# Kernel optimization log

Hardware: AMD Instinct MI355X
Metric: run time of the kernel (lower is better)

## Reference

```python
import jax, jax.numpy as jnp
import numpy as np

E = 512; H = 512; L = 3; NH = 8; HD = H // NH; V = 32000
B = 64; S = 64; T = 20


def setup_inputs() -> dict:
    key = jax.random.key(0)
    ks = jax.random.split(key, 14)
    sc = 0.02
    return {
        "encoder_out": jax.random.normal(ks[0], (B, S, H), jnp.float32),
        "captions": jax.random.randint(ks[1], (B, T), 0, V),
        "embed_table": jax.random.normal(ks[2], (V, E), jnp.float32) * sc,
        "w_ih": jax.random.normal(ks[3], (L, 3 * H, E), jnp.float32) * sc,
        "w_hh": jax.random.normal(ks[4], (L, 3 * H, H), jnp.float32) * sc,
        "b_ih": jax.random.normal(ks[5], (L, 3 * H), jnp.float32) * sc,
        "b_hh": jax.random.normal(ks[6], (L, 3 * H), jnp.float32) * sc,
        "in_proj_w": jax.random.normal(ks[7], (3 * H, H), jnp.float32) * sc,
        "in_proj_b": jax.random.normal(ks[8], (3 * H,), jnp.float32) * sc,
        "out_proj_w": jax.random.normal(ks[9], (H, H), jnp.float32) * sc,
        "out_proj_b": jax.random.normal(ks[10], (H,), jnp.float32) * sc,
        "fc_w": jax.random.normal(ks[11], (V, H), jnp.float32) * sc,
        "fc_b": jax.random.normal(ks[12], (V,), jnp.float32) * sc,
    }


def _gru_cell(x, h, Wih, Whh, bih, bhh):
    # PyTorch GRUCell math. x: (B, in), h: (B, H)
    gi = x @ Wih.T + bih  # (B, 3H)
    gh = h @ Whh.T + bhh
    i_r, i_z, i_n = jnp.split(gi, 3, axis=-1)
    h_r, h_z, h_n = jnp.split(gh, 3, axis=-1)
    r = jax.nn.sigmoid(i_r + h_r)
    z = jax.nn.sigmoid(i_z + h_z)
    n = jnp.tanh(i_n + r * h_n)
    return (1.0 - z) * n + z * h


def reference(encoder_out, captions, embed_table, w_ih, w_hh, b_ih, b_hh,
              in_proj_w, in_proj_b, out_proj_w, out_proj_b, fc_w, fc_b):
    Wq, Wk, Wv = jnp.split(in_proj_w, 3, axis=0)
    bq, bk, bv = jnp.split(in_proj_b, 3, axis=0)
    # K/V projections of encoder_out are timestep-invariant: precompute once.
    Kh = (encoder_out @ Wk.T + bk).reshape(B, S, NH, HD)
    Vh = (encoder_out @ Wv.T + bv).reshape(B, S, NH, HD)
    scale = 1.0 / jnp.sqrt(jnp.float32(HD))

    emb = embed_table[captions]              # (B, T, E)
    xs = jnp.transpose(emb, (1, 0, 2))       # (T, B, E)

    def step(h, x_t):
        # h: (L, B, H); x_t: (B, E)
        new_h = []
        inp = x_t
        for l in range(L):
            hl = _gru_cell(inp, h[l], w_ih[l], w_hh[l], b_ih[l], b_hh[l])
            new_h.append(hl)
            inp = hl
        q = (inp @ Wq.T + bq).reshape(B, NH, HD)
        scores = jnp.einsum('bnd,bsnd->bns', q, Kh) * scale
        attn = jax.nn.softmax(scores, axis=-1)
        ctx = jnp.einsum('bns,bsnd->bnd', attn, Vh).reshape(B, H)
        ao = ctx @ out_proj_w.T + out_proj_b
        logits = ao @ fc_w.T + fc_b           # (B, V)
        return jnp.stack(new_h), logits

    h0 = jnp.zeros((L, B, H), dtype=encoder_out.dtype)
    _, logits = jax.lax.scan(step, h0, xs)    # logits: (T, B, V)
    return jnp.transpose(logits, (1, 0, 2))   # (B, T, V)
```

## Files before the change

### kernel.cpp

```cpp
#include <hip/hip_runtime.h>
#include <hip/hip_bf16.h>

#define TT 20
#define BB 64
#define SS 64
#define HH 512
#define EE 512
#define VV 32000

typedef __bf16 bf16x8 __attribute__((ext_vector_type(8)));
typedef float f32x4 __attribute__((ext_vector_type(4)));


__global__ __launch_bounds__(256) void f2bf_kernel(const float* __restrict__ in,
                                                   __hip_bfloat16* __restrict__ out, int n) {
    int i = blockIdx.x * 256 + threadIdx.x;
    if (i < n) out[i] = __float2bfloat16(in[i]);
}

__global__ __launch_bounds__(256) void zero_h_kernel(float* __restrict__ hf,
                                                     __hip_bfloat16* __restrict__ hb, int n) {
    int i = blockIdx.x * 256 + threadIdx.x;
    if (i < n) { hf[i] = 0.f; hb[i] = __float2bfloat16(0.f); }
}

__global__ __launch_bounds__(256) void gather_emb_kernel(const float* __restrict__ tab,
                                                         const int* __restrict__ cap,
                                                         __hip_bfloat16* __restrict__ out) {
    int i = blockIdx.x * 256 + threadIdx.x;
    int e = i & (EE - 1);
    int tb = i >> 9;
    int t = tb >> 6;
    int b = tb & 63;
    int tok = cap[b * TT + t];
    out[i] = __float2bfloat16(tab[(size_t)tok * EE + e]);
}


__global__ __launch_bounds__(256) void gemm_bt_kernel(
    const __hip_bfloat16* __restrict__ A,
    const __hip_bfloat16* __restrict__ Bm,
    const float* __restrict__ bias,
    float* __restrict__ Cf,
    __hip_bfloat16* __restrict__ Cb,
    int K, int ldc, int row_stride, int row_off,
    long sAz, long sBz, long sCz)
{
    A  += (size_t)blockIdx.z * sAz;
    Bm += (size_t)blockIdx.z * sBz;
    long cbase = (long)blockIdx.z * sCz;

    int m0 = blockIdx.x * 64, n0 = blockIdx.y * 64;
    int wave = threadIdx.x >> 6, lane = threadIdx.x & 63;
    int wm = wave & 1, wn = wave >> 1;
    int row16 = lane & 15, quad = lane >> 4;

    const __hip_bfloat16* a0p = A  + (size_t)(m0 + wm * 32 + row16) * K + quad * 8;
    const __hip_bfloat16* a1p = a0p + (size_t)16 * K;
    const __hip_bfloat16* b0p = Bm + (size_t)(n0 + wn * 32 + row16) * K + quad * 8;
    const __hip_bfloat16* b1p = b0p + (size_t)16 * K;

    f32x4 acc00 = {0.f, 0.f, 0.f, 0.f};
    f32x4 acc01 = {0.f, 0.f, 0.f, 0.f};
    f32x4 acc10 = {0.f, 0.f, 0.f, 0.f};
    f32x4 acc11 = {0.f, 0.f, 0.f, 0.f};

    for (int k = 0; k < K; k += 32) {
        bf16x8 a0 = *reinterpret_cast<const bf16x8*>(a0p + k);
        bf16x8 a1 = *reinterpret_cast<const bf16x8*>(a1p + k);
        bf16x8 b0 = *reinterpret_cast<const bf16x8*>(b0p + k);
        bf16x8 b1 = *reinterpret_cast<const bf16x8*>(b1p + k);
        acc00 = __builtin_amdgcn_mfma_f32_16x16x32_bf16(a0, b0, acc00, 0, 0, 0);
        acc01 = __builtin_amdgcn_mfma_f32_16x16x32_bf16(a0, b1, acc01, 0, 0, 0);
        acc10 = __builtin_amdgcn_mfma_f32_16x16x32_bf16(a1, b0, acc10, 0, 0, 0);
        acc11 = __builtin_amdgcn_mfma_f32_16x16x32_bf16(a1, b1, acc11, 0, 0, 0);
    }

    f32x4 accs[2][2] = {{acc00, acc01}, {acc10, acc11}};
#pragma unroll
    for (int mt = 0; mt < 2; ++mt) {
#pragma unroll
        for (int nt = 0; nt < 2; ++nt) {
            int col = n0 + wn * 32 + nt * 16 + row16;
            float bv = bias ? bias[col] : 0.f;
#pragma unroll
            for (int r = 0; r < 4; ++r) {
                int row = m0 + wm * 32 + mt * 16 + quad * 4 + r;
                long off = cbase + (long)(row * row_stride + row_off) * ldc + col;
                float v = accs[mt][nt][r] + bv;
                if (Cb) Cb[off] = __float2bfloat16(v);
                else    Cf[off] = v;
            }
        }
    }
}


__device__ inline float sigmf(float x) { return 1.f / (1.f + __expf(-x)); }

__global__ __launch_bounds__(256) void gru_combine_kernel(
    const float* __restrict__ GI, const float* __restrict__ GH,
    const float* __restrict__ bih, const float* __restrict__ bhh,
    float* __restrict__ h, __hip_bfloat16* __restrict__ hb)
{
    int i = blockIdx.x * 256 + threadIdx.x;
    int b = i >> 9, j = i & 511;
    const float* gi = GI + (size_t)b * 1536;
    const float* gh = GH + (size_t)b * 1536;
    float ir = gi[j]        + bih[j];
    float iz = gi[j + 512]  + bih[j + 512];
    float in_ = gi[j + 1024] + bih[j + 1024];
    float hr = gh[j]        + bhh[j];
    float hz = gh[j + 512]  + bhh[j + 512];
    float hn = gh[j + 1024] + bhh[j + 1024];
    float r = sigmf(ir + hr);
    float z = sigmf(iz + hz);
    float n = tanhf(in_ + r * hn);
    float hv = h[i];
    float hnew = (1.f - z) * n + z * hv;
    h[i] = hnew;
    hb[i] = __float2bfloat16(hnew);
}

__global__ __launch_bounds__(64) void attn_kernel(
    const float* __restrict__ q, const float* __restrict__ KV,
    __hip_bfloat16* __restrict__ ctxb)
{
    int b = blockIdx.x >> 3, nh = blockIdx.x & 7;
    int lane = threadIdx.x;

    const float* qrow = q + (size_t)b * HH + nh * 64;
    const float* kr   = KV + (size_t)(b * 64 + lane) * 1024 + nh * 64;
    float sc = 0.f;
#pragma unroll
    for (int d = 0; d < 64; ++d) sc += qrow[d] * kr[d];
    sc *= 0.125f;

    float m = sc;
    for (int off = 32; off; off >>= 1) m = fmaxf(m, __shfl_xor(m, off, 64));
    float e = __expf(sc - m);
    float s = e;
    for (int off = 32; off; off >>= 1) s += __shfl_xor(s, off, 64);
    float p = e / s;

    __shared__ float pl[64];
    pl[lane] = p;
    __syncthreads();

    float acc = 0.f;
    const float* vb = KV + (size_t)(b * 64) * 1024 + 512 + nh * 64 + lane;
#pragma unroll
    for (int si = 0; si < 64; ++si) acc += pl[si] * vb[(size_t)si * 1024];

    ctxb[(size_t)b * HH + nh * 64 + lane] = __float2bfloat16(acc);
}


extern "C" void kernel_launch(void* const* d_in, const int* in_sizes, int n_in,
                              void* d_out, int out_size, void* d_ws, size_t ws_size,
                              hipStream_t stream) {
    const float* enc        = (const float*)d_in[0];
    const int*   cap        = (const int*)d_in[1];
    const float* emb_tab    = (const float*)d_in[2];
    const float* w_ih       = (const float*)d_in[3];
    const float* w_hh       = (const float*)d_in[4];
    const float* b_ih       = (const float*)d_in[5];
    const float* b_hh       = (const float*)d_in[6];
    const float* in_proj_w  = (const float*)d_in[7];
    const float* in_proj_b  = (const float*)d_in[8];
    const float* out_proj_w = (const float*)d_in[9];
    const float* out_proj_b = (const float*)d_in[10];
    const float* fc_w       = (const float*)d_in[11];
    const float* fc_b       = (const float*)d_in[12];
    float* out = (float*)d_out;

    char* p = (char*)d_ws;
    auto alloc = [&](size_t bytes) {
        char* r = p;
        p += (bytes + 255) & ~(size_t)255;
        return r;
    };
    __hip_bfloat16* fcw_bf  = (__hip_bfloat16*)alloc((size_t)VV * HH * 2);
    __hip_bfloat16* enc_bf  = (__hip_bfloat16*)alloc((size_t)BB * SS * HH * 2);
    __hip_bfloat16* inp_bf  = (__hip_bfloat16*)alloc((size_t)1536 * 512 * 2);
    __hip_bfloat16* wih_bf  = (__hip_bfloat16*)alloc((size_t)3 * 1536 * 512 * 2);
    __hip_bfloat16* whh_bf  = (__hip_bfloat16*)alloc((size_t)3 * 1536 * 512 * 2);
    __hip_bfloat16* wo_bf   = (__hip_bfloat16*)alloc((size_t)512 * 512 * 2);
    __hip_bfloat16* xemb_bf = (__hip_bfloat16*)alloc((size_t)TT * BB * EE * 2);
    float* KV    = (float*)alloc((size_t)4096 * 1024 * 4);
    float* GI0   = (float*)alloc((size_t)1280 * 1536 * 4);
    float* GH    = (float*)alloc((size_t)3 * 64 * 1536 * 4);
    float* GIbuf = (float*)alloc((size_t)64 * 1536 * 4);
    float* hf    = (float*)alloc((size_t)3 * 64 * 512 * 4);
    __hip_bfloat16* hb     = (__hip_bfloat16*)alloc((size_t)3 * 64 * 512 * 2);
    float* qbuf  = (float*)alloc((size_t)64 * 512 * 4);
    __hip_bfloat16* ctx_bf = (__hip_bfloat16*)alloc((size_t)64 * 512 * 2);
    __hip_bfloat16* AO     = (__hip_bfloat16*)alloc((size_t)1280 * 512 * 2);

    auto cvt = [&](const float* src, __hip_bfloat16* dst, int n) {
        f2bf_kernel<<<(n + 255) / 256, 256, 0, stream>>>(src, dst, n);
    };
    cvt(fc_w, fcw_bf, VV * HH);
    cvt(enc, enc_bf, BB * SS * HH);
    cvt(in_proj_w, inp_bf, 1536 * 512);
    cvt(w_ih, wih_bf, 3 * 1536 * 512);
    cvt(w_hh, whh_bf, 3 * 1536 * 512);
    cvt(out_proj_w, wo_bf, 512 * 512);
    gather_emb_kernel<<<(TT * BB * EE) / 256, 256, 0, stream>>>(emb_tab, cap, xemb_bf);
    zero_h_kernel<<<(3 * 64 * 512) / 256, 256, 0, stream>>>(hf, hb, 3 * 64 * 512);

    gemm_bt_kernel<<<dim3(64, 16, 1), 256, 0, stream>>>(
        enc_bf, inp_bf + 512 * 512, in_proj_b + 512, KV, nullptr,
        512, 1024, 1, 0, 0, 0, 0);

    gemm_bt_kernel<<<dim3(20, 24, 1), 256, 0, stream>>>(
        xemb_bf, wih_bf, nullptr, GI0, nullptr,
        512, 1536, 1, 0, 0, 0, 0);

    for (int t = 0; t < TT; ++t) {
        gemm_bt_kernel<<<dim3(1, 24, 3), 256, 0, stream>>>(
            hb, whh_bf, nullptr, GH, nullptr,
            512, 1536, 1, 0, (long)64 * 512, (long)1536 * 512, (long)64 * 1536);

        gru_combine_kernel<<<128, 256, 0, stream>>>(
            GI0 + (size_t)t * 64 * 1536, GH, b_ih, b_hh, hf, hb);
        gemm_bt_kernel<<<dim3(1, 24, 1), 256, 0, stream>>>(
            hb, wih_bf + (size_t)1 * 1536 * 512, nullptr, GIbuf, nullptr,
            512, 1536, 1, 0, 0, 0, 0);
        gru_combine_kernel<<<128, 256, 0, stream>>>(
            GIbuf, GH + 64 * 1536, b_ih + 1536, b_hh + 1536, hf + 64 * 512, hb + 64 * 512);
        gemm_bt_kernel<<<dim3(1, 24, 1), 256, 0, stream>>>(
            hb + 64 * 512, wih_bf + (size_t)2 * 1536 * 512, nullptr, GIbuf, nullptr,
            512, 1536, 1, 0, 0, 0, 0);
        gru_combine_kernel<<<128, 256, 0, stream>>>(
            GIbuf, GH + 2 * 64 * 1536, b_ih + 2 * 1536, b_hh + 2 * 1536,
            hf + 2 * 64 * 512, hb + 2 * 64 * 512);

        gemm_bt_kernel<<<dim3(1, 8, 1), 256, 0, stream>>>(
            hb + 2 * 64 * 512, inp_bf, in_proj_b, qbuf, nullptr,
            512, 512, 1, 0, 0, 0, 0);

        attn_kernel<<<512, 64, 0, stream>>>(qbuf, KV, ctx_bf);

        gemm_bt_kernel<<<dim3(1, 8, 1), 256, 0, stream>>>(
            ctx_bf, wo_bf, out_proj_b, nullptr, AO,
            512, 512, TT, t, 0, 0, 0);
    }

    gemm_bt_kernel<<<dim3(20, 500, 1), 256, 0, stream>>>(
        AO, fcw_bf, fc_b, out, nullptr,
        512, VV, 1, 0, 0, 0, 0);
}
```

Measured before the change: 1.860 ms.

## Fuse recurrence into persistent grid-barrier kernel and add LDS-tiled 128x128 GEMM

Replaces the roughly 180 per-timestep kernel launches with a single persistent 64-block kernel. It loops over timesteps, uses an atomic grid barrier between stages, fuses each GRU gate GEMM with its elementwise combine, and overlaps the output projection with the next step's layer-0 work. The large GEMMs (KV projection, input gates, vocab projection) now use a new 128x128 tile kernel that stages operands through LDS with async global-to-LDS loads. This targets launch overhead and intermediate round trips through global memory. The cost is spin-wait barriers that depend on all 64 blocks being co-resident, and much less parallelism inside the recurrence.

```diff
diff --git a/kernel.cpp b/kernel.cpp
--- a/kernel.cpp
+++ b/kernel.cpp
@@ -3,13 +3,13 @@
 
 #define TT 20
 #define BB 64
-#define SS 64
 #define HH 512
-#define EE 512
 #define VV 32000
 
 typedef __bf16 bf16x8 __attribute__((ext_vector_type(8)));
 typedef float f32x4 __attribute__((ext_vector_type(4)));
+
+#define MFMA(a, b, c) __builtin_amdgcn_mfma_f32_16x16x32_bf16((a), (b), (c), 0, 0, 0)
 
 
 __global__ __launch_bounds__(256) void f2bf_kernel(const float* __restrict__ in,
@@ -18,141 +18,322 @@
     if (i < n) out[i] = __float2bfloat16(in[i]);
 }
 
-__global__ __launch_bounds__(256) void zero_h_kernel(float* __restrict__ hf,
-                                                     __hip_bfloat16* __restrict__ hb, int n) {
+__global__ __launch_bounds__(256) void init_kernel(float* __restrict__ hf,
+                                                   __hip_bfloat16* __restrict__ hb, int n,
+                                                   unsigned* __restrict__ barcnt) {
     int i = blockIdx.x * 256 + threadIdx.x;
     if (i < n) { hf[i] = 0.f; hb[i] = __float2bfloat16(0.f); }
+    if (i == 0) *barcnt = 0u;
 }
 
 __global__ __launch_bounds__(256) void gather_emb_kernel(const float* __restrict__ tab,
                                                          const int* __restrict__ cap,
                                                          __hip_bfloat16* __restrict__ out) {
     int i = blockIdx.x * 256 + threadIdx.x;
-    int e = i & (EE - 1);
+    int e = i & 511;
     int tb = i >> 9;
     int t = tb >> 6;
     int b = tb & 63;
     int tok = cap[b * TT + t];
-    out[i] = __float2bfloat16(tab[(size_t)tok * EE + e]);
-}
-
-
-__global__ __launch_bounds__(256) void gemm_bt_kernel(
+    out[i] = __float2bfloat16(tab[(size_t)tok * 512 + e]);
+}
+
+
+__device__ inline void async16(const void* g, void* l) {
+    __builtin_amdgcn_global_load_lds(
+        (const __attribute__((address_space(1))) unsigned int*)g,
+        (__attribute__((address_space(3))) unsigned int*)l, 16, 0, 0);
+}
+
+__global__ __launch_bounds__(256) void fastgemm_kernel(
     const __hip_bfloat16* __restrict__ A,
     const __hip_bfloat16* __restrict__ Bm,
     const float* __restrict__ bias,
-    float* __restrict__ Cf,
-    __hip_bfloat16* __restrict__ Cb,
-    int K, int ldc, int row_stride, int row_off,
-    long sAz, long sBz, long sCz)
+    float* __restrict__ C,
+    int K, int N)
 {
-    A  += (size_t)blockIdx.z * sAz;
-    Bm += (size_t)blockIdx.z * sBz;
-    long cbase = (long)blockIdx.z * sCz;
-
-    int m0 = blockIdx.x * 64, n0 = blockIdx.y * 64;
-    int wave = threadIdx.x >> 6, lane = threadIdx.x & 63;
+    __shared__ __align__(16) __hip_bfloat16 lsA[128 * 32];
+    __shared__ __align__(16) __hip_bfloat16 lsB[128 * 32];
+
+    int m0 = blockIdx.x * 128, n0 = blockIdx.y * 128;
+    int tid = threadIdx.x;
+    int wave = tid >> 6, lane = tid & 63, row16 = lane & 15, quad = lane >> 4;
     int wm = wave & 1, wn = wave >> 1;
-    int row16 = lane & 15, quad = lane >> 4;
-
-    const __hip_bfloat16* a0p = A  + (size_t)(m0 + wm * 32 + row16) * K + quad * 8;
-    const __hip_bfloat16* a1p = a0p + (size_t)16 * K;
-    const __hip_bfloat16* b0p = Bm + (size_t)(n0 + wn * 32 + row16) * K + quad * 8;
-    const __hip_bfloat16* b1p = b0p + (size_t)16 * K;
-
-    f32x4 acc00 = {0.f, 0.f, 0.f, 0.f};
-    f32x4 acc01 = {0.f, 0.f, 0.f, 0.f};
-    f32x4 acc10 = {0.f, 0.f, 0.f, 0.f};
-    f32x4 acc11 = {0.f, 0.f, 0.f, 0.f};
-
-    for (int k = 0; k < K; k += 32) {
-        bf16x8 a0 = *reinterpret_cast<const bf16x8*>(a0p + k);
-        bf16x8 a1 = *reinterpret_cast<const bf16x8*>(a1p + k);
-        bf16x8 b0 = *reinterpret_cast<const bf16x8*>(b0p + k);
-        bf16x8 b1 = *reinterpret_cast<const bf16x8*>(b1p + k);
-        acc00 = __builtin_amdgcn_mfma_f32_16x16x32_bf16(a0, b0, acc00, 0, 0, 0);
-        acc01 = __builtin_amdgcn_mfma_f32_16x16x32_bf16(a0, b1, acc01, 0, 0, 0);
-        acc10 = __builtin_amdgcn_mfma_f32_16x16x32_bf16(a1, b0, acc10, 0, 0, 0);
-        acc11 = __builtin_amdgcn_mfma_f32_16x16x32_bf16(a1, b1, acc11, 0, 0, 0);
-    }
-
-    f32x4 accs[2][2] = {{acc00, acc01}, {acc10, acc11}};
-#pragma unroll
-    for (int mt = 0; mt < 2; ++mt) {
-#pragma unroll
-        for (int nt = 0; nt < 2; ++nt) {
-            int col = n0 + wn * 32 + nt * 16 + row16;
+
+    int srow = tid >> 2;
+    int scol = (tid & 3) * 8;
+    const __hip_bfloat16* ga = A + (size_t)(m0 + srow) * K + scol;
+    const __hip_bfloat16* gb = Bm + (size_t)(n0 + srow) * K + scol;
+    __hip_bfloat16* la0 = &lsA[srow * 32 + scol];
+    __hip_bfloat16* la1 = &lsA[(64 + srow) * 32 + scol];
+    __hip_bfloat16* lb0 = &lsB[srow * 32 + scol];
+    __hip_bfloat16* lb1 = &lsB[(64 + srow) * 32 + scol];
+
+    f32x4 acc[4][4] = {};
+
+    for (int kt = 0; kt < K; kt += 32) {
+        async16(ga + kt, la0);
+        async16(ga + kt + (size_t)64 * K, la1);
+        async16(gb + kt, lb0);
+        async16(gb + kt + (size_t)64 * K, lb1);
+        __syncthreads();
+
+        bf16x8 af[4], bfr[4];
+#pragma unroll
+        for (int i = 0; i < 4; ++i)
+            af[i] = *(const bf16x8*)&lsA[(wm * 64 + i * 16 + row16) * 32 + quad * 8];
+#pragma unroll
+        for (int j = 0; j < 4; ++j)
+            bfr[j] = *(const bf16x8*)&lsB[(wn * 64 + j * 16 + row16) * 32 + quad * 8];
+#pragma unroll
+        for (int i = 0; i < 4; ++i)
+#pragma unroll
+            for (int j = 0; j < 4; ++j)
+                acc[i][j] = MFMA(af[i], bfr[j], acc[i][j]);
+        __syncthreads();
+    }
+
+#pragma unroll
+    for (int i = 0; i < 4; ++i)
+#pragma unroll
+        for (int j = 0; j < 4; ++j) {
+            int col = n0 + wn * 64 + j * 16 + row16;
             float bv = bias ? bias[col] : 0.f;
 #pragma unroll
             for (int r = 0; r < 4; ++r) {
-                int row = m0 + wm * 32 + mt * 16 + quad * 4 + r;
-                long off = cbase + (long)(row * row_stride + row_off) * ldc + col;
-                float v = accs[mt][nt][r] + bv;
-                if (Cb) Cb[off] = __float2bfloat16(v);
-                else    Cf[off] = v;
+                int row = m0 + wm * 64 + i * 16 + quad * 4 + r;
+                C[(size_t)row * N + col] = acc[i][j][r] + bv;
             }
         }
-    }
 }
 
 
 __device__ inline float sigmf(float x) { return 1.f / (1.f + __expf(-x)); }
 
-__global__ __launch_bounds__(256) void gru_combine_kernel(
-    const float* __restrict__ GI, const float* __restrict__ GH,
-    const float* __restrict__ bih, const float* __restrict__ bhh,
-    float* __restrict__ h, __hip_bfloat16* __restrict__ hb)
+struct RecArgs {
+    const __hip_bfloat16 *whh, *wih, *wq, *wo;
+    const float *bih, *bhh, *bq, *bo;
+    const float *GI0all;
+    const float *KV;
+    float *hf;
+    __hip_bfloat16 *hb;
+    float *qf;
+    __hip_bfloat16 *ctx;
+    __hip_bfloat16 *AO;
+    unsigned *barcnt;
+};
+
+#define NBLK 64u
+
+__device__ inline void gridbar(unsigned* cnt, unsigned target) {
+    __syncthreads();
+    if (threadIdx.x == 0) {
+        __threadfence();
+        __hip_atomic_fetch_add(cnt, 1u, __ATOMIC_RELAXED, __HIP_MEMORY_SCOPE_AGENT);
+        while (__hip_atomic_load(cnt, __ATOMIC_RELAXED, __HIP_MEMORY_SCOPE_AGENT) < target) {}
+        __threadfence();
+    }
+    __syncthreads();
+}
+
+__device__ inline void gru_stage_l0(
+    const float* __restrict__ GIt, const __hip_bfloat16* __restrict__ A_gh,
+    const __hip_bfloat16* __restrict__ Whh0,
+    const float* __restrict__ bih0, const float* __restrict__ bhh0,
+    const float* __restrict__ hf_in, float* __restrict__ hf_out,
+    __hip_bfloat16* __restrict__ hb_out,
+    int j0, int w, int row16, int quad)
 {
-    int i = blockIdx.x * 256 + threadIdx.x;
-    int b = i >> 9, j = i & 511;
-    const float* gi = GI + (size_t)b * 1536;
-    const float* gh = GH + (size_t)b * 1536;
-    float ir = gi[j]        + bih[j];
-    float iz = gi[j + 512]  + bih[j + 512];
-    float in_ = gi[j + 1024] + bih[j + 1024];
-    float hr = gh[j]        + bhh[j];
-    float hz = gh[j + 512]  + bhh[j + 512];
-    float hn = gh[j + 1024] + bhh[j + 1024];
-    float r = sigmf(ir + hr);
-    float z = sigmf(iz + hz);
-    float n = tanhf(in_ + r * hn);
-    float hv = h[i];
-    float hnew = (1.f - z) * n + z * hv;
-    h[i] = hnew;
-    hb[i] = __float2bfloat16(hnew);
-}
-
-__global__ __launch_bounds__(64) void attn_kernel(
-    const float* __restrict__ q, const float* __restrict__ KV,
-    __hip_bfloat16* __restrict__ ctxb)
+    int koff = quad * 8;
+    const __hip_bfloat16* ah = A_gh + (size_t)(w * 16 + row16) * 512 + koff;
+    const __hip_bfloat16* wh0 = Whh0 + (size_t)(j0 + row16) * 512 + koff;
+    const __hip_bfloat16* wh1 = wh0 + (size_t)512 * 512;
+    const __hip_bfloat16* wh2 = wh1 + (size_t)512 * 512;
+    f32x4 gh0 = {0,0,0,0}, gh1 = {0,0,0,0}, gh2 = {0,0,0,0};
+    for (int k = 0; k < 512; k += 32) {
+        bf16x8 av = *(const bf16x8*)(ah + k);
+        gh0 = MFMA(av, *(const bf16x8*)(wh0 + k), gh0);
+        gh1 = MFMA(av, *(const bf16x8*)(wh1 + k), gh1);
+        gh2 = MFMA(av, *(const bf16x8*)(wh2 + k), gh2);
+    }
+    int j = j0 + row16;
+    float br = bih0[j], bz = bih0[j + 512], bn = bih0[j + 1024];
+    float cr = bhh0[j], cz = bhh0[j + 512], cn = bhh0[j + 1024];
+#pragma unroll
+    for (int r = 0; r < 4; ++r) {
+        int b = w * 16 + quad * 4 + r;
+        float gir = GIt[(size_t)b * 1536 + j];
+        float giz = GIt[(size_t)b * 1536 + j + 512];
+        float gin = GIt[(size_t)b * 1536 + j + 1024];
+        float rg = sigmf(gir + br + gh0[r] + cr);
+        float zg = sigmf(giz + bz + gh1[r] + cz);
+        float ng = tanhf(gin + bn + rg * (gh2[r] + cn));
+        float hv = (1.f - zg) * ng + zg * hf_in[(size_t)b * 512 + j];
+        hf_out[(size_t)b * 512 + j] = hv;
+        hb_out[(size_t)b * 512 + j] = __float2bfloat16(hv);
+    }
+}
+
+__device__ inline void gru_stage_mid(
+    const __hip_bfloat16* __restrict__ A_gi, const __hip_bfloat16* __restrict__ A_gh,
+    const __hip_bfloat16* __restrict__ Wih_l, const __hip_bfloat16* __restrict__ Whh_l,
+    const float* __restrict__ bih_l, const float* __restrict__ bhh_l,
+    const float* __restrict__ hf_in, float* __restrict__ hf_out,
+    __hip_bfloat16* __restrict__ hb_out,
+    int j0, int w, int row16, int quad)
 {
-    int b = blockIdx.x >> 3, nh = blockIdx.x & 7;
-    int lane = threadIdx.x;
-
-    const float* qrow = q + (size_t)b * HH + nh * 64;
-    const float* kr   = KV + (size_t)(b * 64 + lane) * 1024 + nh * 64;
-    float sc = 0.f;
-#pragma unroll
-    for (int d = 0; d < 64; ++d) sc += qrow[d] * kr[d];
-    sc *= 0.125f;
-
-    float m = sc;
-    for (int off = 32; off; off >>= 1) m = fmaxf(m, __shfl_xor(m, off, 64));
-    float e = __expf(sc - m);
-    float s = e;
-    for (int off = 32; off; off >>= 1) s += __shfl_xor(s, off, 64);
-    float p = e / s;
-
-    __shared__ float pl[64];
-    pl[lane] = p;
-    __syncthreads();
-
-    float acc = 0.f;
-    const float* vb = KV + (size_t)(b * 64) * 1024 + 512 + nh * 64 + lane;
-#pragma unroll
-    for (int si = 0; si < 64; ++si) acc += pl[si] * vb[(size_t)si * 1024];
-
-    ctxb[(size_t)b * HH + nh * 64 + lane] = __float2bfloat16(acc);
+    int koff = quad * 8;
+    const __hip_bfloat16* ai = A_gi + (size_t)(w * 16 + row16) * 512 + koff;
+    const __hip_bfloat16* ah = A_gh + (size_t)(w * 16 + row16) * 512 + koff;
+    const __hip_bfloat16* wi0 = Wih_l + (size_t)(j0 + row16) * 512 + koff;
+    const __hip_bfloat16* wi1 = wi0 + (size_t)512 * 512;
+    const __hip_bfloat16* wi2 = wi1 + (size_t)512 * 512;
+    const __hip_bfloat16* wh0 = Whh_l + (size_t)(j0 + row16) * 512 + koff;
+    const __hip_bfloat16* wh1 = wh0 + (size_t)512 * 512;
+    const __hip_bfloat16* wh2 = wh1 + (size_t)512 * 512;
+    f32x4 gi0 = {0,0,0,0}, gi1 = {0,0,0,0}, gi2 = {0,0,0,0};
+    f32x4 gh0 = {0,0,0,0}, gh1 = {0,0,0,0}, gh2 = {0,0,0,0};
+    for (int k = 0; k < 512; k += 32) {
+        bf16x8 av_i = *(const bf16x8*)(ai + k);
+        bf16x8 av_h = *(const bf16x8*)(ah + k);
+        gi0 = MFMA(av_i, *(const bf16x8*)(wi0 + k), gi0);
+        gi1 = MFMA(av_i, *(const bf16x8*)(wi1 + k), gi1);
+        gi2 = MFMA(av_i, *(const bf16x8*)(wi2 + k), gi2);
+        gh0 = MFMA(av_h, *(const bf16x8*)(wh0 + k), gh0);
+        gh1 = MFMA(av_h, *(const bf16x8*)(wh1 + k), gh1);
+        gh2 = MFMA(av_h, *(const bf16x8*)(wh2 + k), gh2);
+    }
+    int j = j0 + row16;
+    float br = bih_l[j], bz = bih_l[j + 512], bn = bih_l[j + 1024];
+    float cr = bhh_l[j], cz = bhh_l[j + 512], cn = bhh_l[j + 1024];
+#pragma unroll
+    for (int r = 0; r < 4; ++r) {
+        int b = w * 16 + quad * 4 + r;
+        float rg = sigmf(gi0[r] + br + gh0[r] + cr);
+        float zg = sigmf(gi1[r] + bz + gh1[r] + cz);
+        float ng = tanhf(gi2[r] + bn + rg * (gh2[r] + cn));
+        float hv = (1.f - zg) * ng + zg * hf_in[(size_t)b * 512 + j];
+        hf_out[(size_t)b * 512 + j] = hv;
+        hb_out[(size_t)b * 512 + j] = __float2bfloat16(hv);
+    }
+}
+
+__device__ inline f32x4 proj16(const __hip_bfloat16* __restrict__ A,
+                               const __hip_bfloat16* __restrict__ Bw,
+                               int w, int row16, int quad)
+{
+    int koff = quad * 8;
+    const __hip_bfloat16* ap = A + (size_t)(w * 16 + row16) * 512 + koff;
+    const __hip_bfloat16* bp = Bw + (size_t)row16 * 512 + koff;
+    f32x4 acc = {0,0,0,0};
+    for (int k = 0; k < 512; k += 32)
+        acc = MFMA(*(const bf16x8*)(ap + k), *(const bf16x8*)(bp + k), acc);
+    return acc;
+}
+
+#define HSTATE (3 * 64 * 512)
+
+__global__ void __launch_bounds__(256, 1) recurrence_kernel(RecArgs a) {
+    const int tid = threadIdx.x;
+    const int blk = blockIdx.x;
+    const int w = tid >> 6, lane = tid & 63, row16 = lane & 15, quad = lane >> 4;
+    unsigned epoch = 0;
+
+    for (int t = 0; t < TT; ++t) {
+        const int cur = t & 1, nxt = cur ^ 1;
+        const __hip_bfloat16* hbc = a.hb + cur * HSTATE;
+        __hip_bfloat16* hbn = a.hb + nxt * HSTATE;
+        const float* hfc = a.hf + cur * HSTATE;
+        float* hfn = a.hf + nxt * HSTATE;
+
+        if (blk < 32) {
+            gru_stage_l0(a.GI0all + (size_t)t * 64 * 1536, hbc, a.whh,
+                         a.bih, a.bhh, hfc, hfn, hbn, blk * 16, w, row16, quad);
+        } else if (t > 0) {
+            int j0 = (blk - 32) * 16;
+            f32x4 acc = proj16(a.ctx, a.wo + (size_t)j0 * 512, w, row16, quad);
+            int j = j0 + row16;
+            float bv = a.bo[j];
+#pragma unroll
+            for (int r = 0; r < 4; ++r) {
+                int b = w * 16 + quad * 4 + r;
+                a.AO[(size_t)(b * TT + (t - 1)) * 512 + j] = __float2bfloat16(acc[r] + bv);
+            }
+        }
+        gridbar(a.barcnt, NBLK * ++epoch);
+
+        if (blk < 32)
+            gru_stage_mid(hbn, hbc + HSTATE / 3,
+                          a.wih + (size_t)1 * 1536 * 512, a.whh + (size_t)1 * 1536 * 512,
+                          a.bih + 1536, a.bhh + 1536,
+                          hfc + HSTATE / 3, hfn + HSTATE / 3, hbn + HSTATE / 3,
+                          blk * 16, w, row16, quad);
+        gridbar(a.barcnt, NBLK * ++epoch);
+
+        if (blk < 32)
+            gru_stage_mid(hbn + HSTATE / 3, hbc + 2 * (HSTATE / 3),
+                          a.wih + (size_t)2 * 1536 * 512, a.whh + (size_t)2 * 1536 * 512,
+                          a.bih + 2 * 1536, a.bhh + 2 * 1536,
+                          hfc + 2 * (HSTATE / 3), hfn + 2 * (HSTATE / 3),
+                          hbn + 2 * (HSTATE / 3),
+                          blk * 16, w, row16, quad);
+        gridbar(a.barcnt, NBLK * ++epoch);
+
+        if (blk < 32) {
+            int j0 = blk * 16;
+            f32x4 acc = proj16(hbn + 2 * (HSTATE / 3), a.wq + (size_t)j0 * 512, w, row16, quad);
+            int j = j0 + row16;
+            float bv = a.bq[j];
+#pragma unroll
+            for (int r = 0; r < 4; ++r) {
+                int b = w * 16 + quad * 4 + r;
+                a.qf[(size_t)b * 512 + j] = acc[r] + bv;
+            }
+        }
+        gridbar(a.barcnt, NBLK * ++epoch);
+
+        {
+            int wg = blk * 4 + w;
+#pragma unroll
+            for (int it = 0; it < 2; ++it) {
+                int task = wg * 2 + it;
+                int b = task >> 3, h = task & 7;
+                const float* qrow = a.qf + (size_t)b * 512 + h * 64;
+                const float* kr = a.KV + (size_t)(b * 64 + lane) * 1024 + h * 64;
+                float sc = 0.f;
+#pragma unroll
+                for (int d = 0; d < 64; ++d) sc += qrow[d] * kr[d];
+                sc *= 0.125f;
+                float m = sc;
+                for (int off = 32; off; off >>= 1) m = fmaxf(m, __shfl_xor(m, off, 64));
+                float e = __expf(sc - m);
+                float s = e;
+                for (int off = 32; off; off >>= 1) s += __shfl_xor(s, off, 64);
+                float p = e / s;
+                float accv = 0.f;
+                const float* vb = a.KV + (size_t)(b * 64) * 1024 + 512 + h * 64 + lane;
+#pragma unroll
+                for (int si = 0; si < 64; ++si) {
+                    float ps = __shfl(p, si, 64);
+                    accv += ps * vb[(size_t)si * 1024];
+                }
+                a.ctx[(size_t)b * 512 + h * 64 + lane] = __float2bfloat16(accv);
+            }
+        }
+        gridbar(a.barcnt, NBLK * ++epoch);
+    }
+
+    if (blk >= 32) {
+        int j0 = (blk - 32) * 16;
+        f32x4 acc = proj16(a.ctx, a.wo + (size_t)j0 * 512, w, row16, quad);
+        int j = j0 + row16;
+        float bv = a.bo[j];
+#pragma unroll
+        for (int r = 0; r < 4; ++r) {
+            int b = w * 16 + quad * 4 + r;
+            a.AO[(size_t)(b * TT + 19) * 512 + j] = __float2bfloat16(acc[r] + bv);
+        }
+    }
 }
 
 
@@ -181,73 +362,47 @@
         return r;
     };
     __hip_bfloat16* fcw_bf  = (__hip_bfloat16*)alloc((size_t)VV * HH * 2);
-    __hip_bfloat16* enc_bf  = (__hip_bfloat16*)alloc((size_t)BB * SS * HH * 2);
+    __hip_bfloat16* enc_bf  = (__hip_bfloat16*)alloc((size_t)64 * 64 * 512 * 2);
     __hip_bfloat16* inp_bf  = (__hip_bfloat16*)alloc((size_t)1536 * 512 * 2);
     __hip_bfloat16* wih_bf  = (__hip_bfloat16*)alloc((size_t)3 * 1536 * 512 * 2);
     __hip_bfloat16* whh_bf  = (__hip_bfloat16*)alloc((size_t)3 * 1536 * 512 * 2);
     __hip_bfloat16* wo_bf   = (__hip_bfloat16*)alloc((size_t)512 * 512 * 2);
-    __hip_bfloat16* xemb_bf = (__hip_bfloat16*)alloc((size_t)TT * BB * EE * 2);
-    float* KV    = (float*)alloc((size_t)4096 * 1024 * 4);
-    float* GI0   = (float*)alloc((size_t)1280 * 1536 * 4);
-    float* GH    = (float*)alloc((size_t)3 * 64 * 1536 * 4);
-    float* GIbuf = (float*)alloc((size_t)64 * 1536 * 4);
-    float* hf    = (float*)alloc((size_t)3 * 64 * 512 * 4);
-    __hip_bfloat16* hb     = (__hip_bfloat16*)alloc((size_t)3 * 64 * 512 * 2);
-    float* qbuf  = (float*)alloc((size_t)64 * 512 * 4);
+    __hip_bfloat16* xemb_bf = (__hip_bfloat16*)alloc((size_t)TT * 64 * 512 * 2);
+    float* KV     = (float*)alloc((size_t)4096 * 1024 * 4);
+    float* GI0all = (float*)alloc((size_t)1280 * 1536 * 4);
+    float* hf     = (float*)alloc((size_t)2 * HSTATE * 4);
+    __hip_bfloat16* hb = (__hip_bfloat16*)alloc((size_t)2 * HSTATE * 2);
+    float* qf     = (float*)alloc((size_t)64 * 512 * 4);
     __hip_bfloat16* ctx_bf = (__hip_bfloat16*)alloc((size_t)64 * 512 * 2);
     __hip_bfloat16* AO     = (__hip_bfloat16*)alloc((size_t)1280 * 512 * 2);
-
-    auto cvt = [&](const float* src, __hip_bfloat16* dst, int n) {
-        f2bf_kernel<<<(n + 255) / 256, 256, 0, stream>>>(src, dst, n);
+    unsigned* barcnt = (unsigned*)alloc(256);
+
+    auto cvt = [&](const float* src, __hip_bfloat16* dst, size_t n) {
+        f2bf_kernel<<<(int)((n + 255) / 256), 256, 0, stream>>>(src, dst, (int)n);
     };
-    cvt(fc_w, fcw_bf, VV * HH);
-    cvt(enc, enc_bf, BB * SS * HH);
-    cvt(in_proj_w, inp_bf, 1536 * 512);
-    cvt(w_ih, wih_bf, 3 * 1536 * 512);
-    cvt(w_hh, whh_bf, 3 * 1536 * 512);
-    cvt(out_proj_w, wo_bf, 512 * 512);
-    gather_emb_kernel<<<(TT * BB * EE) / 256, 256, 0, stream>>>(emb_tab, cap, xemb_bf);
-    zero_h_kernel<<<(3 * 64 * 512) / 256, 256, 0, stream>>>(hf, hb, 3 * 64 * 512);
-
-    gemm_bt_kernel<<<dim3(64, 16, 1), 256, 0, stream>>>(
-        enc_bf, inp_bf + 512 * 512, in_proj_b + 512, KV, nullptr,
-        512, 1024, 1, 0, 0, 0, 0);
-
-    gemm_bt_kernel<<<dim3(20, 24, 1), 256, 0, stream>>>(
-        xemb_bf, wih_bf, nullptr, GI0, nullptr,
-        512, 1536, 1, 0, 0, 0, 0);
-
-    for (int t = 0; t < TT; ++t) {
-        gemm_bt_kernel<<<dim3(1, 24, 3), 256, 0, stream>>>(
-            hb, whh_bf, nullptr, GH, nullptr,
-            512, 1536, 1, 0, (long)64 * 512, (long)1536 * 512, (long)64 * 1536);
-
-        gru_combine_kernel<<<128, 256, 0, stream>>>(
-            GI0 + (size_t)t * 64 * 1536, GH, b_ih, b_hh, hf, hb);
-        gemm_bt_kernel<<<dim3(1, 24, 1), 256, 0, stream>>>(
-            hb, wih_bf + (size_t)1 * 1536 * 512, nullptr, GIbuf, nullptr,
-            512, 1536, 1, 0, 0, 0, 0);
-        gru_combine_kernel<<<128, 256, 0, stream>>>(
-            GIbuf, GH + 64 * 1536, b_ih + 1536, b_hh + 1536, hf + 64 * 512, hb + 64 * 512);
-        gemm_bt_kernel<<<dim3(1, 24, 1), 256, 0, stream>>>(
-            hb + 64 * 512, wih_bf + (size_t)2 * 1536 * 512, nullptr, GIbuf, nullptr,
-            512, 1536, 1, 0, 0, 0, 0);
-        gru_combine_kernel<<<128, 256, 0, stream>>>(
-            GIbuf, GH + 2 * 64 * 1536, b_ih + 2 * 1536, b_hh + 2 * 1536,
-            hf + 2 * 64 * 512, hb + 2 * 64 * 512);
-
-        gemm_bt_kernel<<<dim3(1, 8, 1), 256, 0, stream>>>(
-            hb + 2 * 64 * 512, inp_bf, in_proj_b, qbuf, nullptr,
-            512, 512, 1, 0, 0, 0, 0);
-
-        attn_kernel<<<512, 64, 0, stream>>>(qbuf, KV, ctx_bf);
-
-        gemm_bt_kernel<<<dim3(1, 8, 1), 256, 0, stream>>>(
-            ctx_bf, wo_bf, out_proj_b, nullptr, AO,
-            512, 512, TT, t, 0, 0, 0);
-    }
-
-    gemm_bt_kernel<<<dim3(20, 500, 1), 256, 0, stream>>>(
-        AO, fcw_bf, fc_b, out, nullptr,
-        512, VV, 1, 0, 0, 0, 0);
-}
+    cvt(fc_w, fcw_bf, (size_t)VV * HH);
+    cvt(enc, enc_bf, (size_t)64 * 64 * 512);
+    cvt(in_proj_w, inp_bf, (size_t)1536 * 512);
+    cvt(w_ih, wih_bf, (size_t)3 * 1536 * 512);
+    cvt(w_hh, whh_bf, (size_t)3 * 1536 * 512);
+    cvt(out_proj_w, wo_bf, (size_t)512 * 512);
+    gather_emb_kernel<<<(TT * 64 * 512) / 256, 256, 0, stream>>>(emb_tab, cap, xemb_bf);
+    init_kernel<<<(HSTATE + 255) / 256, 256, 0, stream>>>(hf, hb, HSTATE, barcnt);
+
+    fastgemm_kernel<<<dim3(32, 8), 256, 0, stream>>>(
+        enc_bf, inp_bf + (size_t)512 * 512, in_proj_b + 512, KV, 512, 1024);
+
+    fastgemm_kernel<<<dim3(10, 12), 256, 0, stream>>>(
+        xemb_bf, wih_bf, nullptr, GI0all, 512, 1536);
+
+    RecArgs ra;
+    ra.whh = whh_bf; ra.wih = wih_bf; ra.wq = inp_bf; ra.wo = wo_bf;
+    ra.bih = b_ih; ra.bhh = b_hh; ra.bq = in_proj_b; ra.bo = out_proj_b;
+    ra.GI0all = GI0all; ra.KV = KV;
+    ra.hf = hf; ra.hb = hb; ra.qf = qf; ra.ctx = ctx_bf; ra.AO = AO;
+    ra.barcnt = barcnt;
+    recurrence_kernel<<<dim3(64), dim3(256), 0, stream>>>(ra);
+
+    fastgemm_kernel<<<dim3(10, 250), 256, 0, stream>>>(
+        AO, fcw_bf, fc_b, out, 512, VV);
+}
```

Result: slower. 2.930 ms (+57.5%).
